# Kernel optimization log

Hardware: AMD Instinct MI355X
Metric: run time of the kernel (lower is better)

The kernel has to match this reference:

```python
import jax, jax.numpy as jnp
import numpy as np

EPS = 1e-12  # F.normalize eps

def _l2norm(v, axis):
    n = jnp.sqrt(jnp.sum(v * v, axis=axis, keepdims=True))
    return v / jnp.maximum(n, EPS)

def setup_inputs() -> dict:
    key = jax.random.key(0)
    ks = jax.random.split(key, 4)
    B, N, C, centers = 128, 196, 768, 64
    x = jax.random.normal(ks[0], (B, N, C), dtype=jnp.float32)
    k_c = jax.random.normal(ks[1], (C, centers), dtype=jnp.float32)
    v_c = jax.random.normal(ks[2], (centers, N, N), dtype=jnp.float32)
    proj_w = jax.random.normal(ks[3], (C, C), dtype=jnp.float32) * (C ** -0.5)
    proj_b = jnp.zeros((C,), dtype=jnp.float32)
    return {"x": x, "k_c": k_c, "v_c": v_c, "proj_w": proj_w, "proj_b": proj_b}

def reference(x, k_c, v_c, proj_w, proj_b):
    # x: (B, N, C); k_c: (C, centers); v_c: (centers, N, N)
    C = x.shape[-1]
    scale = C ** -0.5
    q = x.mean(axis=1)                                  # (B, C)
    attn = _l2norm(q, -1) @ _l2norm(k_c, 0)             # (B, centers)
    attn = jax.nn.softmax(attn * scale, axis=-1)        # (B, centers)
    # attention-weighted mixture of basis matrices: (B,centers)x(centers,N*N) GEMM
    v = jnp.einsum('bc,cnm->bnm', attn, v_c)            # (B, N, N)
    out = jnp.einsum('bnm,bmd->bnd', v, x)              # (B, N, C)
    out = out @ proj_w.T + proj_b                        # Linear(dim, dim)
    return out
```

## Files before the change

kernel.cpp:

```cpp
#include <hip/hip_runtime.h>
#include <hip/hip_bf16.h>


#define NB   128
#define NN   196
#define NC   768
#define NCEN 64
#define RPAD 256
#define KPAD 224
#define BGRP 32

using bf16x8 = __attribute__((ext_vector_type(8))) short;
using f32x4  = __attribute__((ext_vector_type(4))) float;

__device__ __forceinline__ void async_copy16(const void* g, void* l) {
    __builtin_amdgcn_global_load_lds((const __attribute__((address_space(1))) void*)g,
                                     (__attribute__((address_space(3))) void*)l, 16, 0, 0);
}

__global__ __launch_bounds__(256)
void convert_x_kernel(const float* __restrict__ x, __hip_bfloat16* __restrict__ x_bf,
                      float* __restrict__ q_part) {
    int b = blockIdx.x, chunk = blockIdx.y, part = blockIdx.z, t = threadIdx.x;
    int c = chunk * 256 + t;
    const float* xp = x + (size_t)b * NN * NC + c;
    __hip_bfloat16* xo = x_bf + (size_t)b * RPAD * NC + c;
    float s = 0.f;
    int m0 = part * 64;
#pragma unroll 4
    for (int m = m0; m < m0 + 64; ++m) {
        if (m < NN) {
            float v = xp[(size_t)m * NC];
            s += v;
            xo[(size_t)m * NC] = __float2bfloat16(v);
        } else {
            xo[(size_t)m * NC] = __float2bfloat16(0.f);
        }
    }
    q_part[((size_t)part * NB + b) * NC + c] = s;
}

__global__ __launch_bounds__(256)
void convert_w_kernel(const float* __restrict__ w, __hip_bfloat16* __restrict__ w_bf) {
    int i = blockIdx.x * 256 + threadIdx.x;
    if (i < NC * NC) w_bf[i] = __float2bfloat16(w[i]);
}

__global__ __launch_bounds__(256)
void attn_kernel(const float* __restrict__ q_part, const float* __restrict__ k_c,
                 float* __restrict__ attn) {
    const float SCALE = 0.03608439182435161f;
    int b = blockIdx.x, t = threadIdx.x;
    __shared__ float qs[NC];
    __shared__ float red[256];
    __shared__ float pd[4][NCEN];
    __shared__ float pk[4][NCEN];

    const size_t PS = (size_t)NB * NC;
    for (int i = t; i < NC; i += 256) {
        size_t idx = (size_t)b * NC + i;
        qs[i] = (q_part[idx] + q_part[PS + idx] + q_part[2 * PS + idx] + q_part[3 * PS + idx])
                * (1.0f / (float)NN);
    }
    __syncthreads();

    float s = 0.f;
    for (int i = t; i < NC; i += 256) { float v = qs[i]; s += v * v; }
    red[t] = s;
    __syncthreads();
    for (int o = 128; o > 0; o >>= 1) {
        if (t < o) red[t] += red[t + o];
        __syncthreads();
    }
    float qn = sqrtf(red[0]);

    int j = t & 63, part = t >> 6;
    float d = 0.f, kk = 0.f;
    int c0 = part * 192;
    for (int c = c0; c < c0 + 192; ++c) {
        float kv = k_c[c * NCEN + j];
        d += kv * qs[c];
        kk += kv * kv;
    }
    pd[part][j] = d;
    pk[part][j] = kk;
    __syncthreads();

    if (t < NCEN) {
        float dot = pd[0][t] + pd[1][t] + pd[2][t] + pd[3][t];
        float kn  = sqrtf(pk[0][t] + pk[1][t] + pk[2][t] + pk[3][t]);
        float lg = dot / (fmaxf(qn, 1e-12f) * fmaxf(kn, 1e-12f)) * SCALE;
        float mx = lg;
        for (int o = 32; o > 0; o >>= 1) mx = fmaxf(mx, __shfl_xor(mx, o, 64));
        float e = expf(lg - mx);
        float sum = e;
        for (int o = 32; o > 0; o >>= 1) sum += __shfl_xor(sum, o, 64);
        attn[b * NCEN + t] = e / sum;
    }
}

__global__ __launch_bounds__(256)
void mix_kernel(const float* __restrict__ attn, const float* __restrict__ v_c,
                __hip_bfloat16* __restrict__ v_pad) {
    int n = blockIdx.x;
    int g = blockIdx.y;
    int m = threadIdx.x;

    __shared__ float sattn[BGRP][NCEN];
    for (int i = threadIdx.x; i < BGRP * NCEN; i += 256)
        sattn[i >> 6][i & 63] = attn[(g * BGRP + (i >> 6)) * NCEN + (i & 63)];
    __syncthreads();

    if (m >= KPAD) return;
    __hip_bfloat16 z = __float2bfloat16(0.f);
    size_t base = (size_t)n * KPAD + m;
    if (n >= NN || m >= NN) {
#pragma unroll
        for (int bb = 0; bb < BGRP; ++bb)
            v_pad[(size_t)(g * BGRP + bb) * RPAD * KPAD + base] = z;
        return;
    }
    float vc[NCEN];
    const float* vp = v_c + (size_t)n * NN + m;
#pragma unroll
    for (int c = 0; c < NCEN; ++c) vc[c] = vp[(size_t)c * NN * NN];
#pragma unroll
    for (int bb = 0; bb < BGRP; ++bb) {
        float acc = 0.f;
#pragma unroll
        for (int c = 0; c < NCEN; ++c) acc += sattn[bb][c] * vc[c];
        v_pad[(size_t)(g * BGRP + bb) * RPAD * KPAD + base] = __float2bfloat16(acc);
    }
}

template <int BK, bool OUT_BF16>
__global__ __launch_bounds__(256)
void gemm_nt(const __hip_bfloat16* __restrict__ A, size_t strideA,
             const __hip_bfloat16* __restrict__ Bm, size_t strideB,
             void* __restrict__ Cout, size_t strideC,
             const float* __restrict__ bias,
             int lda, int ldb, int ldc, int K, int Mstore, int Nstore) {
    int bm = blockIdx.x, bn = blockIdx.y, bb = blockIdx.z;
    const unsigned short* Ab = (const unsigned short*)A + (size_t)bb * strideA + (size_t)bm * 128 * lda;
    const unsigned short* Bb = (const unsigned short*)Bm + (size_t)bb * strideB + (size_t)bn * 128 * ldb;

    __shared__ __align__(16) unsigned short sA[128 * BK];
    __shared__ __align__(16) unsigned short sB[128 * BK];

    int tid = threadIdx.x;
    int wave = tid >> 6, lane = tid & 63;
    int wr = wave >> 1, wc = wave & 1;
    int lrow = lane & 15, quad = lane >> 4;

    constexpr int CH  = BK / 8;
    constexpr int RPI = 64 / CH;
    constexpr int NI  = 32 / RPI;
    int srow = lane / CH;
    int sc   = lane % CH;
    int lc   = (BK == 64) ? (sc ^ (srow & 7)) : sc;

    const unsigned short* ga[NI];
    const unsigned short* gb[NI];
    unsigned short* la[NI];
    unsigned short* lb[NI];
#pragma unroll
    for (int i = 0; i < NI; ++i) {
        int row = wave * 32 + i * RPI + srow;
        ga[i] = Ab + (size_t)row * lda + lc * 8;
        gb[i] = Bb + (size_t)row * ldb + lc * 8;
        la[i] = &sA[(wave * 32 + i * RPI) * BK];
        lb[i] = &sB[(wave * 32 + i * RPI) * BK];
    }

    f32x4 acc[4][4] = {};

    for (int k0 = 0; k0 < K; k0 += BK) {
        __syncthreads();
#pragma unroll
        for (int i = 0; i < NI; ++i) async_copy16(ga[i] + k0, la[i]);
#pragma unroll
        for (int i = 0; i < NI; ++i) async_copy16(gb[i] + k0, lb[i]);
        __syncthreads();

#pragma unroll
        for (int kh = 0; kh < BK / 32; ++kh) {
            int pcbase = (BK == 64) ? ((kh * 4 + quad) ^ (lrow & 7)) : quad;
            bf16x8 af[4], bfr[4];
#pragma unroll
            for (int i = 0; i < 4; ++i)
                af[i] = *(const bf16x8*)(&sA[(wr * 64 + i * 16 + lrow) * BK + pcbase * 8]);
#pragma unroll
            for (int j = 0; j < 4; ++j)
                bfr[j] = *(const bf16x8*)(&sB[(wc * 64 + j * 16 + lrow) * BK + pcbase * 8]);
#pragma unroll
            for (int i = 0; i < 4; ++i)
#pragma unroll
                for (int j = 0; j < 4; ++j)
                    acc[i][j] = __builtin_amdgcn_mfma_f32_16x16x32_bf16(af[i], bfr[j], acc[i][j], 0, 0, 0);
        }
    }

    size_t cbase = (size_t)bb * strideC;
#pragma unroll
    for (int i = 0; i < 4; ++i) {
        int row0 = bm * 128 + wr * 64 + i * 16 + quad * 4;
#pragma unroll
        for (int j = 0; j < 4; ++j) {
            int col = bn * 128 + wc * 64 + j * 16 + lrow;
            if (col < Nstore) {
                float badd = bias ? bias[col] : 0.f;
#pragma unroll
                for (int r = 0; r < 4; ++r) {
                    int row = row0 + r;
                    if (row < Mstore) {
                        float v = acc[i][j][r] + badd;
                        if (OUT_BF16)
                            ((__hip_bfloat16*)Cout)[cbase + (size_t)row * ldc + col] = __float2bfloat16(v);
                        else
                            ((float*)Cout)[cbase + (size_t)row * ldc + col] = v;
                    }
                }
            }
        }
    }
}

extern "C" void kernel_launch(void* const* d_in, const int* in_sizes, int n_in,
                              void* d_out, int out_size, void* d_ws, size_t ws_size,
                              hipStream_t stream) {
    const float* x      = (const float*)d_in[0];
    const float* k_c    = (const float*)d_in[1];
    const float* v_c    = (const float*)d_in[2];
    const float* proj_w = (const float*)d_in[3];
    const float* proj_b = (const float*)d_in[4];
    float* out = (float*)d_out;

    char* ws = (char*)d_ws;
    size_t off = 0;
    auto alloc = [&](size_t bytes) {
        void* p = ws + off;
        off = (off + bytes + 255) & ~(size_t)255;
        return p;
    };
    __hip_bfloat16* x_bf  = (__hip_bfloat16*)alloc((size_t)NB * RPAD * NC * 2);
    __hip_bfloat16* w_bf  = (__hip_bfloat16*)alloc((size_t)NC * NC * 2);
    __hip_bfloat16* xp_t  = (__hip_bfloat16*)alloc((size_t)NB * NC * KPAD * 2);
    __hip_bfloat16* v_pad = (__hip_bfloat16*)alloc((size_t)NB * RPAD * KPAD * 2);
    float* q_part = (float*)alloc((size_t)4 * NB * NC * 4);
    float* attn   = (float*)alloc((size_t)NB * NCEN * 4);

    convert_x_kernel<<<dim3(NB, 3, 4), 256, 0, stream>>>(x, x_bf, q_part);
    convert_w_kernel<<<dim3((NC * NC + 255) / 256), 256, 0, stream>>>(proj_w, w_bf);
    attn_kernel<<<dim3(NB), 256, 0, stream>>>(q_part, k_c, attn);
    mix_kernel<<<dim3(RPAD, NB / BGRP), 256, 0, stream>>>(attn, v_c, v_pad);

    gemm_nt<64, true><<<dim3(6, 2, NB), 256, 0, stream>>>(
        w_bf, 0, x_bf, (size_t)RPAD * NC, xp_t, (size_t)NC * KPAD, nullptr,
        NC, NC, KPAD, NC, NC, KPAD);

    gemm_nt<32, false><<<dim3(2, 6, NB), 256, 0, stream>>>(
        v_pad, (size_t)RPAD * KPAD, xp_t, (size_t)NC * KPAD, out, (size_t)NN * NC, proj_b,
        KPAD, KPAD, NC, KPAD, NN, NC);
}
```

Measured before the change: 319.4 us.

## Remap GEMM blocks per XCD and drop padding writes in convert and mix

Both batched GEMMs move to a 1D grid whose block index is decoded so that consecutive blocks on the same XCD share a batch or weight tile. The aim is better L2 reuse across the XCD-interleaved dispatch. convert_x now splits the 196 rows into four 49-row parts and no longer writes zero padding rows. mix_kernel launches only 196 row blocks and reads attn straight from global memory instead of staging it in shared memory. The skipped zero writes rely on the workspace padding in x_bf being harmless: rows 196..255 are no longer zeroed, and garbage (e.g. NaN) there could leak through multiplications by zero.

After: 324.6 us. Within noise of the previous version (+1.6%).

```diff
diff --git a/kernel.cpp b/kernel.cpp
--- a/kernel.cpp
+++ b/kernel.cpp
@@ -26,16 +26,12 @@
     const float* xp = x + (size_t)b * NN * NC + c;
     __hip_bfloat16* xo = x_bf + (size_t)b * RPAD * NC + c;
     float s = 0.f;
-    int m0 = part * 64;
-#pragma unroll 4
-    for (int m = m0; m < m0 + 64; ++m) {
-        if (m < NN) {
-            float v = xp[(size_t)m * NC];
-            s += v;
-            xo[(size_t)m * NC] = __float2bfloat16(v);
-        } else {
-            xo[(size_t)m * NC] = __float2bfloat16(0.f);
-        }
+    int m0 = part * 49;
+#pragma unroll 7
+    for (int m = m0; m < m0 + 49; ++m) {
+        float v = xp[(size_t)m * NC];
+        s += v;
+        xo[(size_t)m * NC] = __float2bfloat16(v);
     }
     q_part[((size_t)part * NB + b) * NC + c] = s;
 }
@@ -105,16 +101,10 @@
     int n = blockIdx.x;
     int g = blockIdx.y;
     int m = threadIdx.x;
-
-    __shared__ float sattn[BGRP][NCEN];
-    for (int i = threadIdx.x; i < BGRP * NCEN; i += 256)
-        sattn[i >> 6][i & 63] = attn[(g * BGRP + (i >> 6)) * NCEN + (i & 63)];
-    __syncthreads();
-
     if (m >= KPAD) return;
-    __hip_bfloat16 z = __float2bfloat16(0.f);
     size_t base = (size_t)n * KPAD + m;
-    if (n >= NN || m >= NN) {
+    if (m >= NN) {
+        __hip_bfloat16 z = __float2bfloat16(0.f);
 #pragma unroll
         for (int bb = 0; bb < BGRP; ++bb)
             v_pad[(size_t)(g * BGRP + bb) * RPAD * KPAD + base] = z;
@@ -124,23 +114,35 @@
     const float* vp = v_c + (size_t)n * NN + m;
 #pragma unroll
     for (int c = 0; c < NCEN; ++c) vc[c] = vp[(size_t)c * NN * NN];
-#pragma unroll
+    const float* ab = attn + (size_t)g * BGRP * NCEN;
     for (int bb = 0; bb < BGRP; ++bb) {
         float acc = 0.f;
 #pragma unroll
-        for (int c = 0; c < NCEN; ++c) acc += sattn[bb][c] * vc[c];
+        for (int c = 0; c < NCEN; ++c) acc += ab[bb * NCEN + c] * vc[c];
         v_pad[(size_t)(g * BGRP + bb) * RPAD * KPAD + base] = __float2bfloat16(acc);
     }
 }
 
-template <int BK, bool OUT_BF16>
+template <int BK, bool OUT_BF16, int MODE>
 __global__ __launch_bounds__(256)
 void gemm_nt(const __hip_bfloat16* __restrict__ A, size_t strideA,
              const __hip_bfloat16* __restrict__ Bm, size_t strideB,
              void* __restrict__ Cout, size_t strideC,
              const float* __restrict__ bias,
              int lda, int ldb, int ldc, int K, int Mstore, int Nstore) {
-    int bm = blockIdx.x, bn = blockIdx.y, bb = blockIdx.z;
+    int id = blockIdx.x;
+    int bm, bn, bb;
+    if (MODE == 0) {
+        int xcd = id & 7, idx = id >> 3;
+        bm = idx % 6;
+        int grp = xcd * 32 + idx / 6;
+        bn = grp & 1; bb = grp >> 1;
+    } else {
+        int xcd = id & 7, idx = id >> 3;
+        bb = xcd * 16 + idx / 12;
+        int r = idx % 12;
+        bm = r & 1; bn = r >> 1;
+    }
     const unsigned short* Ab = (const unsigned short*)A + (size_t)bb * strideA + (size_t)bm * 128 * lda;
     const unsigned short* Bb = (const unsigned short*)Bm + (size_t)bb * strideB + (size_t)bn * 128 * ldb;
 
@@ -252,13 +254,13 @@
     convert_x_kernel<<<dim3(NB, 3, 4), 256, 0, stream>>>(x, x_bf, q_part);
     convert_w_kernel<<<dim3((NC * NC + 255) / 256), 256, 0, stream>>>(proj_w, w_bf);
     attn_kernel<<<dim3(NB), 256, 0, stream>>>(q_part, k_c, attn);
-    mix_kernel<<<dim3(RPAD, NB / BGRP), 256, 0, stream>>>(attn, v_c, v_pad);
-
-    gemm_nt<64, true><<<dim3(6, 2, NB), 256, 0, stream>>>(
+    mix_kernel<<<dim3(NN, NB / BGRP), 256, 0, stream>>>(attn, v_c, v_pad);
+
+    gemm_nt<64, true, 0><<<dim3(1536), 256, 0, stream>>>(
         w_bf, 0, x_bf, (size_t)RPAD * NC, xp_t, (size_t)NC * KPAD, nullptr,
         NC, NC, KPAD, NC, NC, KPAD);
 
-    gemm_nt<32, false><<<dim3(2, 6, NB), 256, 0, stream>>>(
+    gemm_nt<32, false, 1><<<dim3(1536), 256, 0, stream>>>(
         v_pad, (size_t)RPAD * KPAD, xp_t, (size_t)NC * KPAD, out, (size_t)NN * NC, proj_b,
         KPAD, KPAD, NC, KPAD, NN, NC);
 }
```
